# Kernel tuning notes

Measured on AMD Instinct MI355X. Metric: run time of the kernel, lower is better.

Reference implementation:

```python
import jax, jax.numpy as jnp
import numpy as np

NEG_SLOPE = 0.2  # PyG GATConv default negative_slope


def _gat_layer(x, src, dst, W, a_src, a_dst, b, num_nodes):
    # x: [N, Fin] -> h: [N, Fout]
    h = x @ W
    # per-node attention logits (heads=1)
    alpha_s = h @ a_src  # [N]
    alpha_d = h @ a_dst  # [N]
    # edge scores e_ij = LeakyReLU(a_src . h_j + a_dst . h_i), j=src, i=dst
    e = alpha_s[src] + alpha_d[dst]
    e = jnp.where(e >= 0, e, NEG_SLOPE * e)
    # segment softmax over edges sharing the same destination node
    e_max = jax.ops.segment_max(e, dst, num_segments=num_nodes)  # [N]
    w = jnp.exp(e - e_max[dst])  # [E]
    denom = jax.ops.segment_sum(w, dst, num_segments=num_nodes)  # [N]
    alpha = w / denom[dst]  # [E]
    # weighted scatter-sum of source messages into destinations
    out = jax.ops.segment_sum(h[src] * alpha[:, None], dst, num_segments=num_nodes)
    return out + b


def _add_self_loops(edge_index, num_nodes):
    loops = jnp.arange(num_nodes, dtype=edge_index.dtype)
    src = jnp.concatenate([edge_index[0], loops])
    dst = jnp.concatenate([edge_index[1], loops])
    return src, dst


def setup_inputs() -> dict:
    key = jax.random.key(0)
    ks = jax.random.split(key, 8)
    N, E, F_in, F_hid, F_out = 50000, 800000, 128, 128, 64
    inp = {
        "node_features": jax.random.normal(ks[0], (N, F_in), dtype=jnp.float32),
        "edge_index": jax.random.randint(ks[1], (2, E), 0, N, dtype=jnp.int32),
        "W1": jax.random.normal(ks[2], (F_in, F_hid), dtype=jnp.float32) / np.sqrt(F_in),
        "a_src1": jax.random.normal(ks[3], (F_hid,), dtype=jnp.float32) / np.sqrt(F_hid),
        "a_dst1": jax.random.normal(ks[4], (F_hid,), dtype=jnp.float32) / np.sqrt(F_hid),
        "b1": jnp.zeros((F_hid,), dtype=jnp.float32),
        "W2": jax.random.normal(ks[5], (F_hid, F_out), dtype=jnp.float32) / np.sqrt(F_hid),
        "a_src2": jax.random.normal(ks[6], (F_out,), dtype=jnp.float32) / np.sqrt(F_out),
        "a_dst2": jax.random.normal(ks[7], (F_out,), dtype=jnp.float32) / np.sqrt(F_out),
        "b2": jnp.zeros((F_out,), dtype=jnp.float32),
    }
    return inp


def reference(node_features, edge_index, W1, a_src1, a_dst1, b1, W2, a_src2, a_dst2, b2):
    num_nodes = node_features.shape[0]
    src, dst = _add_self_loops(edge_index, num_nodes)
    x = _gat_layer(node_features, src, dst, W1, a_src1, a_dst1, b1, num_nodes)
    x = jax.nn.relu(x)
    x = _gat_layer(x, src, dst, W2, a_src2, a_dst2, b2, num_nodes)
    return x
```

## Files before the change

kernel.cpp:

```cpp
#include <hip/hip_runtime.h>
#include <hip/hip_fp16.h>
#include <cstddef>

#define NEG_SLOPE 0.2f
#define TILE 4096
#define CSR_CAP 6144

typedef _Float16 h8 __attribute__((ext_vector_type(8)));
typedef _Float16 h4 __attribute__((ext_vector_type(4)));
typedef float f4 __attribute__((ext_vector_type(4)));

__device__ __forceinline__ float leaky(float x) { return x >= 0.f ? x : NEG_SLOPE * x; }

__device__ __forceinline__ int wave_iscan(int v, int lane) {
#pragma unroll
    for (int off = 1; off < 64; off <<= 1) {
        int t = __shfl_up(v, off);
        if (lane >= off) v += t;
    }
    return v;
}

__global__ __launch_bounds__(256) void gemm1_scatter(
    const float* __restrict__ x, const float* __restrict__ W,
    const float* __restrict__ a_s, const float* __restrict__ a_d,
    _Float16* __restrict__ hh, float* __restrict__ alphaS, float* __restrict__ alphaD,
    int N, int nblk_gemm,
    const int* __restrict__ src, const int* __restrict__ dst,
    int* __restrict__ bfill, unsigned* __restrict__ staging, int cap, int E)
{
    constexpr int K = 128;
    constexpr int LDK = K + 8;
    constexpr int F = 128;
    constexpr int NT = F / 16;

    __shared__ union {
        struct { _Float16 As[64 * LDK]; _Float16 Wt[F * LDK]; } g;
        struct {
            int lcnt[256]; int loff[256]; int gbase[256]; int ws[4];
            unsigned pairs[TILE]; unsigned char bkt[TILE];
        } s;
    } u;

    const int tid = threadIdx.x;

    if (blockIdx.x < (unsigned)nblk_gemm) {
        const int wave = tid >> 6;
        const int lane = tid & 63;
        const int q = lane >> 4;
        const int c = lane & 15;
        const int rowb = blockIdx.x * 64;

        for (int i = tid; i < 64 * (K / 4); i += 256) {
            int r = i >> 5, c4 = i & 31;
            int gr = rowb + r;
            float4 v = (gr < N) ? *(const float4*)(x + (size_t)gr * K + c4 * 4)
                                : make_float4(0.f, 0.f, 0.f, 0.f);
            h4 hv = { (_Float16)v.x, (_Float16)v.y, (_Float16)v.z, (_Float16)v.w };
            *(h4*)(u.g.As + r * LDK + c4 * 4) = hv;
        }
        for (int i = tid; i < K * F; i += 256) {
            int k = i / F, n = i % F;
            u.g.Wt[n * LDK + k] = (_Float16)W[i];
        }
        __syncthreads();

        f4 acc[NT];
#pragma unroll
        for (int nt = 0; nt < NT; nt++) acc[nt] = (f4)0.f;

        const _Float16* aw = u.g.As + (wave * 16 + c) * LDK + q * 8;
#pragma unroll
        for (int kt = 0; kt < 4; kt++) {
            h8 af = *(const h8*)(aw + kt * 32);
#pragma unroll
            for (int nt = 0; nt < NT; nt++) {
                h8 bf = *(const h8*)(u.g.Wt + (nt * 16 + c) * LDK + kt * 32 + q * 8);
                acc[nt] = __builtin_amdgcn_mfma_f32_16x16x32_f16(af, bf, acc[nt], 0, 0, 0);
            }
        }

        float asl[NT], adl[NT];
#pragma unroll
        for (int nt = 0; nt < NT; nt++) {
            asl[nt] = a_s[nt * 16 + c];
            adl[nt] = a_d[nt * 16 + c];
        }
        const int row0 = rowb + wave * 16 + q * 4;
#pragma unroll
        for (int r = 0; r < 4; r++) {
            int row = row0 + r;
            if (row < N) {
                float ps = 0.f, pd = 0.f;
#pragma unroll
                for (int nt = 0; nt < NT; nt++) {
                    float v = acc[nt][r];
                    hh[(size_t)row * F + nt * 16 + c] = (_Float16)v;
                    ps += v * asl[nt];
                    pd += v * adl[nt];
                }
#pragma unroll
                for (int off = 8; off >= 1; off >>= 1) {
                    ps += __shfl_down(ps, off, 16);
                    pd += __shfl_down(pd, off, 16);
                }
                if (c == 0) { alphaS[row] = ps; alphaD[row] = pd; }
            }
        }
    } else {
        const int base = (blockIdx.x - nblk_gemm) * TILE;
        const int vt = min(TILE, E - base);

        u.s.lcnt[tid] = 0;
        __syncthreads();

        int d[TILE / 256], s[TILE / 256], r[TILE / 256];
#pragma unroll
        for (int j = 0; j < TILE / 256; j++) {
            int idx = base + j * 256 + tid;
            if (idx < E) {
                d[j] = dst[idx]; s[j] = src[idx];
                r[j] = atomicAdd(&u.s.lcnt[d[j] >> 8], 1);
            } else d[j] = -1;
        }
        __syncthreads();
        {
            int lane = tid & 63, wid = tid >> 6;
            int v = u.s.lcnt[tid];
            int incl = wave_iscan(v, lane);
            if (lane == 63) u.s.ws[wid] = incl;
            __syncthreads();
            int woff = 0;
            for (int w = 0; w < wid; w++) woff += u.s.ws[w];
            u.s.loff[tid] = woff + incl - v;
        }
        __syncthreads();
        {
            int c = u.s.lcnt[tid];
            if (c > 0) u.s.gbase[tid] = tid * cap + atomicAdd(&bfill[tid], c);
        }
        __syncthreads();
#pragma unroll
        for (int j = 0; j < TILE / 256; j++) {
            if (d[j] >= 0) {
                int b = d[j] >> 8;
                int slot = u.s.loff[b] + r[j];
                u.s.pairs[slot] = ((unsigned)d[j] << 16) | (unsigned)s[j];
                u.s.bkt[slot] = (unsigned char)b;
            }
        }
        __syncthreads();
        for (int slot = tid; slot < vt; slot += 256) {
            int b = u.s.bkt[slot];
            staging[u.s.gbase[b] + (slot - u.s.loff[b])] = u.s.pairs[slot];
        }
    }
}

template <int F, typename IT>
__global__ __launch_bounds__(256) void gemm_mfma(
    const IT* __restrict__ x, const float* __restrict__ W,
    const float* __restrict__ a_s, const float* __restrict__ a_d,
    _Float16* __restrict__ hh, float* __restrict__ alphaS, float* __restrict__ alphaD,
    int N)
{
    constexpr int K = 128;
    constexpr int LDK = K + 8;
    constexpr int NT = F / 16;

    __shared__ _Float16 As[64 * LDK];
    __shared__ _Float16 Wt[F * LDK];

    const int tid = threadIdx.x;
    const int wave = tid >> 6;
    const int lane = tid & 63;
    const int q = lane >> 4;
    const int c = lane & 15;
    const int rowb = blockIdx.x * 64;

    if constexpr (sizeof(IT) == 4) {
        for (int i = tid; i < 64 * (K / 4); i += 256) {
            int r = i >> 5, c4 = i & 31;
            int gr = rowb + r;
            float4 v = (gr < N) ? *(const float4*)((const float*)x + (size_t)gr * K + c4 * 4)
                                : make_float4(0.f, 0.f, 0.f, 0.f);
            h4 hv = { (_Float16)v.x, (_Float16)v.y, (_Float16)v.z, (_Float16)v.w };
            *(h4*)(As + r * LDK + c4 * 4) = hv;
        }
    } else {
        for (int i = tid; i < 64 * (K / 8); i += 256) {
            int r = i >> 4, c8 = i & 15;
            int gr = rowb + r;
            h8 v;
            if (gr < N) v = *(const h8*)((const _Float16*)x + (size_t)gr * K + c8 * 8);
            else        v = (h8)(_Float16)0.f;
            *(h8*)(As + r * LDK + c8 * 8) = v;
        }
    }
    for (int i = tid; i < K * F; i += 256) {
        int k = i / F, n = i % F;
        Wt[n * LDK + k] = (_Float16)W[i];
    }
    __syncthreads();

    f4 acc[NT];
#pragma unroll
    for (int nt = 0; nt < NT; nt++) acc[nt] = (f4)0.f;

    const _Float16* aw = As + (wave * 16 + c) * LDK + q * 8;
#pragma unroll
    for (int kt = 0; kt < 4; kt++) {
        h8 af = *(const h8*)(aw + kt * 32);
#pragma unroll
        for (int nt = 0; nt < NT; nt++) {
            h8 bf = *(const h8*)(Wt + (nt * 16 + c) * LDK + kt * 32 + q * 8);
            acc[nt] = __builtin_amdgcn_mfma_f32_16x16x32_f16(af, bf, acc[nt], 0, 0, 0);
        }
    }

    float asl[NT], adl[NT];
#pragma unroll
    for (int nt = 0; nt < NT; nt++) {
        asl[nt] = a_s[nt * 16 + c];
        adl[nt] = a_d[nt * 16 + c];
    }
    const int row0 = rowb + wave * 16 + q * 4;
#pragma unroll
    for (int r = 0; r < 4; r++) {
        int row = row0 + r;
        if (row < N) {
            float ps = 0.f, pd = 0.f;
#pragma unroll
            for (int nt = 0; nt < NT; nt++) {
                float v = acc[nt][r];
                hh[(size_t)row * F + nt * 16 + c] = (_Float16)v;
                ps += v * asl[nt];
                pd += v * adl[nt];
            }
#pragma unroll
            for (int off = 8; off >= 1; off >>= 1) {
                ps += __shfl_down(ps, off, 16);
                pd += __shfl_down(pd, off, 16);
            }
            if (c == 0) { alphaS[row] = ps; alphaD[row] = pd; }
        }
    }
}

__global__ __launch_bounds__(256) void bucket_to_csr(
    const unsigned* __restrict__ staging, const int* __restrict__ bfill,
    int* __restrict__ row_start, int* __restrict__ row_end,
    int* __restrict__ src_sorted, int cap, int N)
{
    __shared__ unsigned lp[CSR_CAP];
    __shared__ int lcnt[256], loff[256], lfill[256];
    __shared__ int ws[4];
    const int tid = threadIdx.x;
    const int b = blockIdx.x;
    const int beg = b * cap;
    const int len = bfill[b];

    lcnt[tid] = 0;
    __syncthreads();
    for (int p = tid; p < len; p += 256) {
        unsigned u = staging[beg + p];
        if (p < CSR_CAP) lp[p] = u;
        atomicAdd(&lcnt[(u >> 16) & 255], 1);
    }
    __syncthreads();
    {
        int lane = tid & 63, wid = tid >> 6;
        int v = lcnt[tid];
        int incl = wave_iscan(v, lane);
        if (lane == 63) ws[wid] = incl;
        __syncthreads();
        int woff = 0;
        for (int w = 0; w < wid; w++) woff += ws[w];
        int excl = woff + incl - v;
        loff[tid] = excl;
        lfill[tid] = excl;
        int node = (b << 8) + tid;
        if (node < N) { row_start[node] = beg + excl; row_end[node] = beg + excl + v; }
    }
    __syncthreads();
    for (int p = tid; p < len; p += 256) {
        unsigned u = (p < CSR_CAP) ? lp[p] : staging[beg + p];
        int pos = atomicAdd(&lfill[(u >> 16) & 255], 1);
        src_sorted[beg + pos] = (int)(u & 0xFFFFu);
    }
}

template <int F, bool RELU, typename OT>
__global__ __launch_bounds__(256) void gat_aggregate(
    const int* __restrict__ row_start, const int* __restrict__ row_end,
    const int* __restrict__ src_sorted, const __half* __restrict__ hh,
    const float* __restrict__ aS, const float* __restrict__ aD,
    const float* __restrict__ bias, OT* __restrict__ out, int N)
{
    constexpr int LPE = F / 8;
    constexpr int EPW = 64 / LPE;

    const int i = blockIdx.x * 4 + (threadIdx.x >> 6);
    if (i >= N) return;
    const int lane = threadIdx.x & 63;
    const int sub = lane / LPE;
    const int l = lane % LPE;

    const float adi = aD[i];
    const int start = row_start[i];
    const int end = row_end[i];

    float accA[8], accB[8];
#pragma unroll
    for (int q = 0; q < 8; q++) { accA[q] = 0.f; accB[q] = 0.f; }
    float denA = 0.f, denB = 0.f;

    int e = start + sub;
    int s0 = (e + 0 * EPW < end) ? src_sorted[e + 0 * EPW] : -1;
    int s1 = (e + 1 * EPW < end) ? src_sorted[e + 1 * EPW] : -1;
    int s2 = (e + 2 * EPW < end) ? src_sorted[e + 2 * EPW] : -1;
    int s3 = (e + 3 * EPW < end) ? src_sorted[e + 3 * EPW] : -1;

    while (s0 >= 0) {
        int eb = e + 4 * EPW;
        int n0 = (eb + 0 * EPW < end) ? src_sorted[eb + 0 * EPW] : -1;
        int n1 = (eb + 1 * EPW < end) ? src_sorted[eb + 1 * EPW] : -1;
        int n2 = (eb + 2 * EPW < end) ? src_sorted[eb + 2 * EPW] : -1;
        int n3 = (eb + 3 * EPW < end) ? src_sorted[eb + 3 * EPW] : -1;

        {
            float w = __expf(leaky(aS[s0] + adi));
            uint4 u = *(const uint4*)(hh + (size_t)s0 * F + l * 8);
            const __half2* hp = (const __half2*)&u;
#pragma unroll
            for (int q = 0; q < 4; q++) {
                float2 f = __half22float2(hp[q]);
                accA[q * 2] += w * f.x; accA[q * 2 + 1] += w * f.y;
            }
            denA += w;
        }
        if (s1 >= 0) {
            float w = __expf(leaky(aS[s1] + adi));
            uint4 u = *(const uint4*)(hh + (size_t)s1 * F + l * 8);
            const __half2* hp = (const __half2*)&u;
#pragma unroll
            for (int q = 0; q < 4; q++) {
                float2 f = __half22float2(hp[q]);
                accB[q * 2] += w * f.x; accB[q * 2 + 1] += w * f.y;
            }
            denB += w;
        }
        if (s2 >= 0) {
            float w = __expf(leaky(aS[s2] + adi));
            uint4 u = *(const uint4*)(hh + (size_t)s2 * F + l * 8);
            const __half2* hp = (const __half2*)&u;
#pragma unroll
            for (int q = 0; q < 4; q++) {
                float2 f = __half22float2(hp[q]);
                accA[q * 2] += w * f.x; accA[q * 2 + 1] += w * f.y;
            }
            denA += w;
        }
        if (s3 >= 0) {
            float w = __expf(leaky(aS[s3] + adi));
            uint4 u = *(const uint4*)(hh + (size_t)s3 * F + l * 8);
            const __half2* hp = (const __half2*)&u;
#pragma unroll
            for (int q = 0; q < 4; q++) {
                float2 f = __half22float2(hp[q]);
                accB[q * 2] += w * f.x; accB[q * 2 + 1] += w * f.y;
            }
            denB += w;
        }
        e = eb;
        s0 = n0; s1 = n1; s2 = n2; s3 = n3;
    }

    float acc[8];
#pragma unroll
    for (int q = 0; q < 8; q++) acc[q] = accA[q] + accB[q];
    float denom = denA + denB;

#pragma unroll
    for (int off = 32; off >= LPE; off >>= 1) {
#pragma unroll
        for (int q = 0; q < 8; q++) acc[q] += __shfl_down(acc[q], off);
        denom += __shfl_down(denom, off);
    }

    if (sub == 0) {
        float wsf = __expf(leaky(aS[i] + adi));
        uint4 u = *(const uint4*)(hh + (size_t)i * F + l * 8);
        const __half2* hp = (const __half2*)&u;
        float inv = 1.f / (denom + wsf);
        float4 b0 = *(const float4*)(bias + l * 8);
        float4 b1 = *(const float4*)(bias + l * 8 + 4);
        float o[8];
#pragma unroll
        for (int q = 0; q < 4; q++) {
            float2 f = __half22float2(hp[q]);
            o[q * 2]     = (acc[q * 2]     + wsf * f.x) * inv;
            o[q * 2 + 1] = (acc[q * 2 + 1] + wsf * f.y) * inv;
        }
        o[0] += b0.x; o[1] += b0.y; o[2] += b0.z; o[3] += b0.w;
        o[4] += b1.x; o[5] += b1.y; o[6] += b1.z; o[7] += b1.w;
        if (RELU) {
#pragma unroll
            for (int q = 0; q < 8; q++) o[q] = fmaxf(o[q], 0.f);
        }
        if constexpr (sizeof(OT) == 2) {
            __half2 qh[4];
            qh[0] = __floats2half2_rn(o[0], o[1]);
            qh[1] = __floats2half2_rn(o[2], o[3]);
            qh[2] = __floats2half2_rn(o[4], o[5]);
            qh[3] = __floats2half2_rn(o[6], o[7]);
            *(uint4*)((__half*)out + (size_t)i * F + l * 8) = *(uint4*)qh;
        } else {
            *(float4*)((float*)out + (size_t)i * F + l * 8)     = make_float4(o[0], o[1], o[2], o[3]);
            *(float4*)((float*)out + (size_t)i * F + l * 8 + 4) = make_float4(o[4], o[5], o[6], o[7]);
        }
    }
}

extern "C" void kernel_launch(void* const* d_in, const int* in_sizes, int n_in,
                              void* d_out, int out_size, void* d_ws, size_t ws_size,
                              hipStream_t stream)
{
    const float* x   = (const float*)d_in[0];
    const int*   ei  = (const int*)d_in[1];
    const float* W1  = (const float*)d_in[2];
    const float* aS1 = (const float*)d_in[3];
    const float* aD1 = (const float*)d_in[4];
    const float* b1  = (const float*)d_in[5];
    const float* W2  = (const float*)d_in[6];
    const float* aS2 = (const float*)d_in[7];
    const float* aD2 = (const float*)d_in[8];
    const float* b2  = (const float*)d_in[9];

    const int K = 128, F1 = 128, F2 = 64;
    const int N = in_sizes[0] / K;
    const int E = in_sizes[1] / 2;
    const int* src = ei;
    const int* dst = ei + E;

    const int Np = (N + 4) & ~3;
    const int NB = (N + 255) >> 8;
    const int nbt = (E + TILE - 1) / TILE;
    const int nblk_gemm = (N + 63) / 64;
    int cap = (((E / NB) * 3) / 2 + 255) & ~255;
    if (cap > CSR_CAP) cap = CSR_CAP;

    char* wsb = (char*)d_ws;
    int* bfill        = (int*)wsb;      wsb += 256 * 4;
    int* row_start    = (int*)wsb;      wsb += (size_t)Np * 4;
    int* row_end      = (int*)wsb;      wsb += (size_t)Np * 4;
    unsigned* staging = (unsigned*)wsb; wsb += (size_t)NB * CSR_CAP * 4;
    int* src_sorted   = (int*)wsb;      wsb += (size_t)NB * CSR_CAP * 4;
    _Float16* hh1     = (_Float16*)wsb; wsb += (size_t)N * F1 * 2;
    _Float16* x2h     = (_Float16*)wsb; wsb += (size_t)N * F1 * 2;
    _Float16* hh2     = (_Float16*)wsb; wsb += (size_t)N * F2 * 2;
    float* as_        = (float*)wsb;    wsb += (size_t)Np * 4;
    float* ad_        = (float*)wsb;    wsb += (size_t)Np * 4;

    hipMemsetAsync(bfill, 0, 256 * 4, stream);

    dim3 blk(256);

    gemm1_scatter<<<dim3(nblk_gemm + nbt), blk, 0, stream>>>(
        x, W1, aS1, aD1, hh1, as_, ad_, N, nblk_gemm,
        src, dst, bfill, staging, cap, E);

    bucket_to_csr<<<dim3(NB), blk, 0, stream>>>(staging, bfill, row_start, row_end,
                                                src_sorted, cap, N);

    gat_aggregate<F1, true, __half><<<dim3((N + 3) / 4), blk, 0, stream>>>(
        row_start, row_end, src_sorted, (const __half*)hh1, as_, ad_, b1,
        (__half*)x2h, N);

    gemm_mfma<F2, _Float16><<<dim3((N + 63) / 64), blk, 0, stream>>>(
        x2h, W2, aS2, aD2, hh2, as_, ad_, N);

    gat_aggregate<F2, false, float><<<dim3((N + 3) / 4), blk, 0, stream>>>(
        row_start, row_end, src_sorted, (const __half*)hh2, as_, ad_, b2,
        (float*)d_out, N);
}
```

Before: 197.4 us.

## Pre-transpose weights to fp16 once and widen CSR bucket kernel to 512 threads

A small prep kernel converts W1 and W2 to fp16 and transposes them into workspace, and it also zeroes the bucket counters, replacing the memset. Each GEMM block then loads the weights with vectorized 16-byte copies instead of strided scalar fp32 reads with conversion. The bucket-to-CSR kernel now runs 512 threads per block and always reads entries from LDS, dropping the staging fallback. This relies on the bucket length never exceeding CSR_CAP. The cost is one extra kernel launch.

```diff
diff --git a/kernel.cpp b/kernel.cpp
--- a/kernel.cpp
+++ b/kernel.cpp
@@ -21,8 +21,30 @@
     return v;
 }
 
+__global__ __launch_bounds__(256) void prep(
+    const float* __restrict__ W1, const float* __restrict__ W2,
+    _Float16* __restrict__ W1t, _Float16* __restrict__ W2t,
+    int* __restrict__ bfill)
+{
+    const int b = blockIdx.x;
+    const int tid = threadIdx.x;
+    if (b == 0) bfill[tid] = 0;
+    if (b < 8) {
+        for (int i = b * 2048 + tid; i < (b + 1) * 2048; i += 256) {
+            int n = i >> 7, k = i & 127;
+            W1t[n * 128 + k] = (_Float16)W1[k * 128 + n];
+        }
+    } else {
+        const int bb = b - 8;
+        for (int i = bb * 2048 + tid; i < (bb + 1) * 2048; i += 256) {
+            int n = i >> 7, k = i & 127;
+            W2t[n * 128 + k] = (_Float16)W2[k * 64 + n];
+        }
+    }
+}
+
 __global__ __launch_bounds__(256) void gemm1_scatter(
-    const float* __restrict__ x, const float* __restrict__ W,
+    const float* __restrict__ x, const _Float16* __restrict__ Wg,
     const float* __restrict__ a_s, const float* __restrict__ a_d,
     _Float16* __restrict__ hh, float* __restrict__ alphaS, float* __restrict__ alphaD,
     int N, int nblk_gemm,
@@ -59,9 +81,9 @@
             h4 hv = { (_Float16)v.x, (_Float16)v.y, (_Float16)v.z, (_Float16)v.w };
             *(h4*)(u.g.As + r * LDK + c4 * 4) = hv;
         }
-        for (int i = tid; i < K * F; i += 256) {
-            int k = i / F, n = i % F;
-            u.g.Wt[n * LDK + k] = (_Float16)W[i];
+        for (int i = tid; i < F * (K / 8); i += 256) {
+            int n = i >> 4, k8 = i & 15;
+            *(h8*)(u.g.Wt + n * LDK + k8 * 8) = *(const h8*)(Wg + n * 128 + k8 * 8);
         }
         __syncthreads();
 
@@ -159,7 +181,7 @@
 
 template <int F, typename IT>
 __global__ __launch_bounds__(256) void gemm_mfma(
-    const IT* __restrict__ x, const float* __restrict__ W,
+    const IT* __restrict__ x, const _Float16* __restrict__ Wg,
     const float* __restrict__ a_s, const float* __restrict__ a_d,
     _Float16* __restrict__ hh, float* __restrict__ alphaS, float* __restrict__ alphaD,
     int N)
@@ -197,9 +219,9 @@
             *(h8*)(As + r * LDK + c8 * 8) = v;
         }
     }
-    for (int i = tid; i < K * F; i += 256) {
-        int k = i / F, n = i % F;
-        Wt[n * LDK + k] = (_Float16)W[i];
+    for (int i = tid; i < F * (K / 8); i += 256) {
+        int n = i >> 4, k8 = i & 15;
+        *(h8*)(Wt + n * LDK + k8 * 8) = *(const h8*)(Wg + n * 128 + k8 * 8);
     }
     __syncthreads();
 
@@ -247,7 +269,7 @@
     }
 }
 
-__global__ __launch_bounds__(256) void bucket_to_csr(
+__global__ __launch_bounds__(512) void bucket_to_csr(
     const unsigned* __restrict__ staging, const int* __restrict__ bfill,
     int* __restrict__ row_start, int* __restrict__ row_end,
     int* __restrict__ src_sorted, int cap, int N)
@@ -260,31 +282,36 @@
     const int beg = b * cap;
     const int len = bfill[b];
 
-    lcnt[tid] = 0;
+    if (tid < 256) lcnt[tid] = 0;
     __syncthreads();
-    for (int p = tid; p < len; p += 256) {
+    for (int p = tid; p < len; p += 512) {
         unsigned u = staging[beg + p];
-        if (p < CSR_CAP) lp[p] = u;
+        lp[p] = u;
         atomicAdd(&lcnt[(u >> 16) & 255], 1);
     }
     __syncthreads();
     {
         int lane = tid & 63, wid = tid >> 6;
-        int v = lcnt[tid];
-        int incl = wave_iscan(v, lane);
-        if (lane == 63) ws[wid] = incl;
-        __syncthreads();
-        int woff = 0;
-        for (int w = 0; w < wid; w++) woff += ws[w];
-        int excl = woff + incl - v;
-        loff[tid] = excl;
-        lfill[tid] = excl;
-        int node = (b << 8) + tid;
-        if (node < N) { row_start[node] = beg + excl; row_end[node] = beg + excl + v; }
+        int v = 0, incl = 0;
+        if (tid < 256) {
+            v = lcnt[tid];
+            incl = wave_iscan(v, lane);
+            if (lane == 63) ws[wid] = incl;
+        }
+        __syncthreads();
+        if (tid < 256) {
+            int woff = 0;
+            for (int w = 0; w < wid; w++) woff += ws[w];
+            int excl = woff + incl - v;
+            loff[tid] = excl;
+            lfill[tid] = excl;
+            int node = (b << 8) + tid;
+            if (node < N) { row_start[node] = beg + excl; row_end[node] = beg + excl + v; }
+        }
     }
     __syncthreads();
-    for (int p = tid; p < len; p += 256) {
-        unsigned u = (p < CSR_CAP) ? lp[p] : staging[beg + p];
+    for (int p = tid; p < len; p += 512) {
+        unsigned u = lp[p];
         int pos = atomicAdd(&lfill[(u >> 16) & 255], 1);
         src_sorted[beg + pos] = (int)(u & 0xFFFFu);
     }
@@ -452,6 +479,8 @@
 
     char* wsb = (char*)d_ws;
     int* bfill        = (int*)wsb;      wsb += 256 * 4;
+    _Float16* W1t     = (_Float16*)wsb; wsb += 128 * 128 * 2;
+    _Float16* W2t     = (_Float16*)wsb; wsb += 64 * 128 * 2;
     int* row_start    = (int*)wsb;      wsb += (size_t)Np * 4;
     int* row_end      = (int*)wsb;      wsb += (size_t)Np * 4;
     unsigned* staging = (unsigned*)wsb; wsb += (size_t)NB * CSR_CAP * 4;
@@ -462,23 +491,23 @@
     float* as_        = (float*)wsb;    wsb += (size_t)Np * 4;
     float* ad_        = (float*)wsb;    wsb += (size_t)Np * 4;
 
-    hipMemsetAsync(bfill, 0, 256 * 4, stream);
-
     dim3 blk(256);
 
+    prep<<<dim3(12), blk, 0, stream>>>(W1, W2, W1t, W2t, bfill);
+
     gemm1_scatter<<<dim3(nblk_gemm + nbt), blk, 0, stream>>>(
-        x, W1, aS1, aD1, hh1, as_, ad_, N, nblk_gemm,
+        x, W1t, aS1, aD1, hh1, as_, ad_, N, nblk_gemm,
         src, dst, bfill, staging, cap, E);
 
-    bucket_to_csr<<<dim3(NB), blk, 0, stream>>>(staging, bfill, row_start, row_end,
-                                                src_sorted, cap, N);
+    bucket_to_csr<<<dim3(NB), dim3(512), 0, stream>>>(staging, bfill, row_start, row_end,
+                                                      src_sorted, cap, N);
 
     gat_aggregate<F1, true, __half><<<dim3((N + 3) / 4), blk, 0, stream>>>(
         row_start, row_end, src_sorted, (const __half*)hh1, as_, ad_, b1,
         (__half*)x2h, N);
 
     gemm_mfma<F2, _Float16><<<dim3((N + 63) / 64), blk, 0, stream>>>(
-        x2h, W2, aS2, aD2, hh2, as_, ad_, N);
+        x2h, W2t, aS2, aD2, hh2, as_, ad_, N);
 
     gat_aggregate<F2, false, float><<<dim3((N + 3) / 4), blk, 0, stream>>>(
         row_start, row_end, src_sorted, (const __half*)hh2, as_, ad_, b2,
```

Result: faster. 190.9 us (-3.3%).
